# Kernel optimization log

Hardware: AMD Instinct MI355X
Metric: run time of the kernel (lower is better)

## Reference

```python
import jax, jax.numpy as jnp
import numpy as np

N_NODES = 1024
N_FEAT = 12        # must equal LOOKBACK (U1 @ B @ U2.T constraint in original code)
LOOKBACK = 12
N_DATA = 8
KSIZE = 2
DILATIONS = [1, 3, 3, 3]
DELTA_MIN = 0.05
TIME_FEATS = 36    # 15 + 5 + 4 + 12


def setup_inputs() -> dict:
    key = jax.random.key(0)
    ks = jax.random.split(key, 21)
    f32 = jnp.float32

    def rn(k, shape, fan_in):
        return jax.random.normal(k, shape, dtype=f32) / np.sqrt(fan_in)

    return {
        'observation': jax.random.normal(ks[0], (N_NODES, N_DATA, LOOKBACK), dtype=f32),
        'time_features': jax.random.normal(ks[1], (TIME_FEATS,), dtype=f32),
        # main FC stack: (n_nodes*n_data) -> fc1 -> fc2 -> n_nodes*n_feat
        'fc_w1': rn(ks[2], (N_NODES * N_DATA, 2048), N_NODES * N_DATA),
        'fc_b1': jnp.zeros((2048,), f32),
        'fc_w2': rn(ks[3], (2048, 2048), 2048),
        'fc_b2': jnp.zeros((2048,), f32),
        'fc_w3': rn(ks[4], (2048, N_NODES * N_FEAT), 2048),
        'fc_b3': jnp.zeros((N_NODES * N_FEAT,), f32),
        # graph conv weights
        'W_forward': rn(ks[5], (KSIZE, N_FEAT, N_FEAT), N_FEAT),
        'W_backward': rn(ks[6], (KSIZE, N_FEAT, N_FEAT), N_FEAT),
        'b': jnp.zeros((N_FEAT,), f32),
        # GraphConstructor params (one fixed set, reused for every adjacency)
        'layer_initial': rn(ks[7], (LOOKBACK, N_NODES), N_NODES),
        'gs_w1': rn(ks[8], (N_NODES, 256), N_NODES),
        'gs_b1': jnp.zeros((256,), f32),
        'gs_w2': rn(ks[9], (256, N_NODES * N_FEAT), 256),
        'gs_b2': jnp.zeros((N_NODES * N_FEAT,), f32),
        'gt_w1': rn(ks[10], (TIME_FEATS, 256), TIME_FEATS),
        'gt_b1': jnp.zeros((256,), f32),
        'gt_w2': rn(ks[11], (256, N_NODES * N_FEAT), 256),
        'gt_b2': jnp.zeros((N_NODES * N_FEAT,), f32),
        'B': jax.random.normal(ks[12], (N_FEAT, N_FEAT), dtype=f32) / N_FEAT,
    }


def _forward(observation, time_features, fc_w1, fc_b1, fc_w2, fc_b2, fc_w3, fc_b3,
             W_forward, W_backward, b, layer_initial,
             gs_w1, gs_b1, gs_w2, gs_b2, gt_w1, gt_b1, gt_w2, gt_b2, B):
    relu = jax.nn.relu

    # fully_connected: observation (N, D, L) -> X (N, F, L)
    obs = jnp.transpose(observation, (2, 0, 1)).reshape(LOOKBACK, -1)  # (L, N*D)
    h = relu(obs @ fc_w1 + fc_b1)
    h = relu(h @ fc_w2 + fc_b2)
    h = relu(h @ fc_w3 + fc_b3)                                        # (L, N*F)
    X0 = jnp.transpose(h.reshape(LOOKBACK, N_NODES, N_FEAT), (1, 2, 0))  # (N, F, L)

    # node embedding U (N, L, F), computed once (graph params fixed)
    sp = relu(relu(layer_initial @ gs_w1 + gs_b1) @ gs_w2 + gs_b2)     # (L, N*F)
    tp = relu(relu(time_features @ gt_w1 + gt_b1) @ gt_w2 + gt_b2)     # (N*F,)
    U = jnp.transpose((sp + tp).reshape(LOOKBACK, N_NODES, N_FEAT), (1, 0, 2))

    adj_cache = {}

    def norm_adj(a, c):
        # normalized adjacency between feature-slices a and c (static ints)
        if (a, c) in adj_cache:
            return adj_cache[(a, c)]
        U1 = U[:, :, a]                      # (N, L)
        U2 = U[:, :, c]                      # (N, L)
        x = U1 @ B @ U2.T                    # (N, N); valid since L == F
        x = jnp.where(x >= DELTA_MIN, x, 0.0)
        A = jax.nn.softmax(x, axis=1)        # torch F.softmax default dim=1 for 2D
        # degree = diag(rowsum); inv(sqrtm(diag)) = diag(1/sqrt(rowsum))
        d = 1.0 / jnp.sqrt(A.sum(-1))
        out = A * d[:, None] * d[None, :]
        adj_cache[(a, c)] = out
        return out

    def conv(X, t):
        Z = jnp.zeros((N_NODES, N_FEAT), jnp.float32)
        for k in range(KSIZE):
            X_t = X[:, :, t - k]             # (N, F)
            L1 = norm_adj(t - k, t)
            L2 = norm_adj(t + k, t)
            x = L1 @ X_t @ W_forward[k] + L2 @ X_t @ W_backward[k] + b
            Z = Z + jax.nn.relu(x)
        return Z

    def conv_layer(X, d):
        cols = []
        for t in range(1, LOOKBACK - 1):
            if t % d == 0:
                cols.append(conv(X, t))
            else:
                cols.append(jnp.zeros((N_NODES, N_FEAT), jnp.float32))
        return jnp.stack(cols, axis=-1)      # (N, F, L-2)

    Z0 = conv_layer(X0, DILATIONS[0])
    Z1 = conv_layer(Z0, DILATIONS[1])
    Z2 = conv_layer(Z1, DILATIONS[2])
    Z3 = conv_layer(Z2, DILATIONS[3])
    return (Z0[:, :, -1], Z1[:, :, -1], Z2[:, :, -1], Z3[:, :, -1])


def reference(observation, time_features, fc_w1, fc_b1, fc_w2, fc_b2, fc_w3, fc_b3,
              W_forward, W_backward, b, layer_initial,
              gs_w1, gs_b1, gs_w2, gs_b2, gt_w1, gt_b1, gt_w2, gt_b2, B):
    return _forward(observation, time_features, fc_w1, fc_b1, fc_w2, fc_b2, fc_w3, fc_b3,
                    W_forward, W_backward, b, layer_initial,
                    gs_w1, gs_b1, gs_w2, gs_b2, gt_w1, gt_b1, gt_w2, gt_b2, B)
```

## Files before the change

### kernel.cpp

```cpp
#include <hip/hip_runtime.h>

#define OFF_SPP   0
#define OFF_TPH   49152
#define OFF_P1    65536
#define OFF_P2    196608
#define OFF_P3    262144
#define OFF_UP    393216
#define OFF_TPP   1572864
#define OFF_U     1703936

template<int KS, int PIN, int P, int GATHER>
__device__ __forceinline__ void gemm_body(
    const float* __restrict__ xin, const float* __restrict__ bias_in,
    const float* __restrict__ W, float* __restrict__ part,
    int N, int K, int bx, int by, float* lx, float* red)
{
  int tid = threadIdx.x;
  int k0 = by * KS;
  for (int i = tid; i < 2*KS; i += 256) {
    int t = i / KS, kk = i - t*KS;
    float v;
    if (GATHER) {
      int k = k0 + kk;
      v = xin[(k >> 3)*96 + (k & 7)*12 + 9 + t];
    } else if (PIN == 0) {
      v = xin[t*K + k0 + kk];
    } else {
      v = 0.f;
      const float* p0 = xin + (size_t)(t*K + k0 + kk)*PIN;
      #pragma unroll
      for (int pp = 0; pp < PIN; ++pp) v += p0[pp];
    }
    if (bias_in) { v += bias_in[k0 + kk]; v = v > 0.f ? v : 0.f; }
    lx[i] = v;
  }
  __syncthreads();
  int kg = tid >> 5, cg2 = tid & 31;
  int colbase = bx*128 + cg2*4;
  float a0=0,a1=0,a2=0,a3=0,c0=0,c1=0,c2=0,c3=0;
  const int ksub = KS/8;
  for (int kk = kg*ksub; kk < kg*ksub + ksub; ++kk) {
    float4 w = *(const float4*)(W + (size_t)(k0+kk)*N + colbase);
    float x0 = lx[kk], x1 = lx[KS + kk];
    a0=fmaf(x0,w.x,a0); a1=fmaf(x0,w.y,a1); a2=fmaf(x0,w.z,a2); a3=fmaf(x0,w.w,a3);
    c0=fmaf(x1,w.x,c0); c1=fmaf(x1,w.y,c1); c2=fmaf(x1,w.z,c2); c3=fmaf(x1,w.w,c3);
  }
  float* rp = red + (kg*32 + cg2)*8;
  rp[0]=a0; rp[1]=a1; rp[2]=a2; rp[3]=a3; rp[4]=c0; rp[5]=c1; rp[6]=c2; rp[7]=c3;
  __syncthreads();
  int cg3 = tid & 31, q = tid >> 5;
  float s = 0.f;
  #pragma unroll
  for (int g = 0; g < 8; ++g) s += red[(g*32 + cg3)*8 + q];
  int t = q >> 2, c = q & 3;
  part[(size_t)(t*N + bx*128 + cg3*4 + c)*P + by] = s;
}

__global__ void __launch_bounds__(256) k_front(
    const float* __restrict__ obs, const float* __restrict__ fc_w1,
    float* __restrict__ part1,
    const float* __restrict__ li, const float* __restrict__ gs_w1,
    const float* __restrict__ tf, const float* __restrict__ gt_w1,
    const float* __restrict__ gt_b1,
    float* __restrict__ sp_part, float* __restrict__ tp_h,
    float* __restrict__ out_tail)
{
  __shared__ float smem[2560];
  int b = blockIdx.x, tid = threadIdx.x;
  if (b < 512) {
    gemm_body<256, 0, 32, 1>(obs, (const float*)nullptr, fc_w1, part1,
                             2048, 8192, b & 15, b >> 4, smem, smem + 512);
  } else if (b < 528) {
    float (*lil)[128] = (float(*)[128])smem;
    int sb = b - 512;
    int cb = sb & 1, kc = sb >> 1;
    for (int i = tid; i < 1536; i += 256) {
      int r = i >> 7, kk = i & 127;
      lil[r][kk] = li[r*1024 + kc*128 + kk];
    }
    __syncthreads();
    int col = cb*128 + (tid & 127);
    int kh = tid >> 7;
    float acc[12];
    #pragma unroll
    for (int t=0;t<12;++t) acc[t]=0.f;
    for (int kk = kh*64; kk < kh*64 + 64; ++kk) {
      float w = gs_w1[(size_t)(kc*128 + kk)*256 + col];
      #pragma unroll
      for (int t=0;t<12;++t) acc[t] = fmaf(lil[t][kk], w, acc[t]);
    }
    int c = kc*2 + kh;
    #pragma unroll
    for (int t=0;t<12;++t) sp_part[(c*12 + t)*256 + col] = acc[t];
    for (int i = tid; i < 2304; i += 256) out_tail[sb*2304 + i] = 0.f;
  } else {
    float acc = 0.f;
    for (int k = 0; k < 36; ++k)
      acc = fmaf(tf[k], gt_w1[k*256 + tid], acc);
    float v = acc + gt_b1[tid];
    tp_h[tid] = v > 0.f ? v : 0.f;
  }
}

__global__ void __launch_bounds__(256) k_umid(
    const float* __restrict__ part1, const float* __restrict__ fc_b1,
    const float* __restrict__ fc_w2, float* __restrict__ part2,
    const float* __restrict__ sp_part, const float* __restrict__ gs_b1,
    const float* __restrict__ tp_h,
    const float* __restrict__ gs_w2, const float* __restrict__ gt_w2,
    float* __restrict__ U_part, float* __restrict__ tp_part)
{
  __shared__ float smem[2304];
  int b = blockIdx.x, tid = threadIdx.x;
  if (b < 256) {
    gemm_body<128, 32, 16, 0>(part1, fc_b1, fc_w2, part2, 2048, 2048,
                              b & 15, b >> 4, smem, smem + 256);
    return;
  }
  float* spl = smem;
  float* tpl = smem + 96;
  int ug = b - 256;
  int n  = (ug & 3)*256 + tid;
  int uy = ug >> 2;
  int k0 = uy*8;
  if (tid < 96) {
    int kk = tid / 12, t = tid % 12;
    float v = gs_b1[k0 + kk];
    #pragma unroll
    for (int c = 0; c < 16; ++c) v += sp_part[(c*12 + t)*256 + k0 + kk];
    spl[kk*12 + t] = v > 0.f ? v : 0.f;
  }
  if (tid < 8) tpl[tid] = tp_h[k0 + tid];
  __syncthreads();
  float sA[3][12];
  float tA[3] = {0.f, 0.f, 0.f};
  #pragma unroll
  for (int ap=0;ap<3;++ap)
    #pragma unroll
    for (int t=0;t<12;++t) sA[ap][t]=0.f;
  #pragma unroll
  for (int kk = 0; kk < 8; ++kk) {
    float4 ws4 = *(const float4*)(gs_w2 + (size_t)(k0+kk)*12288 + 12*n + 8);
    float4 wt4 = *(const float4*)(gt_w2 + (size_t)(k0+kk)*12288 + 12*n + 8);
    float w0 = ws4.y, w1 = ws4.z, w2 = ws4.w;
    #pragma unroll
    for (int t=0;t<12;++t) {
      float s = spl[kk*12 + t];
      sA[0][t] = fmaf(s, w0, sA[0][t]);
      sA[1][t] = fmaf(s, w1, sA[1][t]);
      sA[2][t] = fmaf(s, w2, sA[2][t]);
    }
    float tv = tpl[kk];
    tA[0] = fmaf(tv, wt4.y, tA[0]);
    tA[1] = fmaf(tv, wt4.z, tA[1]);
    tA[2] = fmaf(tv, wt4.w, tA[2]);
  }
  #pragma unroll
  for (int ap=0;ap<3;++ap) {
    #pragma unroll
    for (int t=0;t<12;++t)
      U_part[(size_t)uy*36864 + ap*12288 + n*12 + t] = sA[ap][t];
    tp_part[uy*3072 + n*3 + ap] = tA[ap];
  }
}

__global__ void __launch_bounds__(256) k_fc3u(
    const float* __restrict__ part2, const float* __restrict__ fc_b2,
    const float* __restrict__ fc_w3, float* __restrict__ part3,
    const float* __restrict__ U_part, const float* __restrict__ tp_part,
    const float* __restrict__ gs_b2, const float* __restrict__ gt_b2,
    float* __restrict__ U)
{
  __shared__ float smem[3072];
  int b = blockIdx.x, tid = threadIdx.x;
  if (b < 384) {
    gemm_body<512, 16, 4, 0>(part2, fc_b2, fc_w3, part3, 12288, 2048,
                             b >> 2, b & 3, smem, smem + 1024);
    return;
  }
  int i = (b - 384)*256 + tid;
  float us = 0.f;
  for (int y = 0; y < 32; ++y) us += U_part[(size_t)y*36864 + i];
  int ap = i / 12288, rem = i - ap*12288, n = rem / 12;
  float ts = 0.f;
  for (int y = 0; y < 32; ++y) ts += tp_part[y*3072 + n*3 + ap];
  int c = n*12 + 9 + ap;
  float sv = us + gs_b2[c]; sv = sv > 0.f ? sv : 0.f;
  float tv = ts + gt_b2[c]; tv = tv > 0.f ? tv : 0.f;
  U[i] = sv + tv;
}

#define SS 1032
__global__ void __launch_bounds__(256) k_final(
    const float* __restrict__ U, const float* __restrict__ Bm,
    const float* __restrict__ part3, const float* __restrict__ fc_b3,
    const float* __restrict__ Wf, const float* __restrict__ Wb,
    const float* __restrict__ bvec, float* __restrict__ out)
{
  __shared__ float sc[6*SS];
  __shared__ float Pm[72];
  __shared__ float invS[6];
  __shared__ float Bl[144];
  __shared__ float Ws0[144], Ws1[144], Ws2[144];
  __shared__ float wbuf[72];
  __shared__ float bl[12];
  int tid = threadIdx.x;
  int i0 = blockIdx.x*2;
  if (tid < 144) {
    Bl[tid]  = Bm[tid];
    Ws0[tid] = Wf[144 + tid];
    Ws1[tid] = Wf[tid] + Wb[tid];
    Ws2[tid] = Wb[144 + tid];
  }
  if (tid < 12) bl[tid] = bvec[tid];
  __syncthreads();
  if (tid < 72) {
    int r = tid / 36, ap = (tid / 12) % 3, j = tid % 12;
    float s = 0.f;
    #pragma unroll
    for (int t=0;t<12;++t)
      s = fmaf(U[ap*12288 + (i0+r)*12 + t], Bl[t*12 + j], s);
    Pm[(r*3+ap)*12 + j] = s;
  }
  __syncthreads();
  const float* U10 = U + 12288;
  for (int jj = 0; jj < 4; ++jj) {
    int j = tid + jj*256;
    const float4* ur = (const float4*)(U10 + j*12);
    float4 u0 = ur[0], u1 = ur[1], u2 = ur[2];
    float u[12] = {u0.x,u0.y,u0.z,u0.w,u1.x,u1.y,u1.z,u1.w,u2.x,u2.y,u2.z,u2.w};
    #pragma unroll
    for (int r=0;r<2;++r)
      #pragma unroll
      for (int ap=0;ap<3;++ap) {
        float s = 0.f;
        #pragma unroll
        for (int t=0;t<12;++t) s = fmaf(Pm[(r*3+ap)*12 + t], u[t], s);
        sc[(r*3+ap)*SS + j] = (s >= 0.05f) ? s : 0.f;
      }
  }
  __syncthreads();
  int wv = tid >> 6, ln = tid & 63;
  for (int pr = wv; pr < 6; pr += 4) {
    float m = -1e30f;
    for (int q = 0; q < 16; ++q) m = fmaxf(m, sc[pr*SS + ln + q*64]);
    #pragma unroll
    for (int o = 32; o > 0; o >>= 1) m = fmaxf(m, __shfl_xor(m, o));
    float sum = 0.f;
    for (int q = 0; q < 16; ++q) {
      int j = ln + q*64;
      float e = __expf(sc[pr*SS + j] - m);
      sc[pr*SS + j] = e;
      sum += e;
    }
    #pragma unroll
    for (int o = 32; o > 0; o >>= 1) sum += __shfl_xor(sum, o);
    if (ln == 0) invS[pr] = 1.f / sum;
  }
  __syncthreads();
  float acc[2][12];
  #pragma unroll
  for (int r = 0; r < 2; ++r)
    #pragma unroll
    for (int f = 0; f < 12; ++f)
      acc[r][f] = 0.f;
  int q3 = tid >> 6, jg = tid & 63;
  if (tid < 192) {
    int row = (q3 == 1) ? 1 : 0;
    const float* p3r = part3 + (size_t)row*49152;
    for (int q = 0; q < 16; ++q) {
      int j = jg + q*64;
      float e0 = sc[q3*SS + j];
      float e1 = sc[(3 + q3)*SS + j];
      const float4* px = (const float4*)(p3r + (size_t)j*48);
      const float* bb = fc_b3 + j*12;
      #pragma unroll
      for (int f = 0; f < 12; ++f) {
        float4 v4 = px[f];
        float x = v4.x + v4.y + v4.z + v4.w + bb[f];
        x = x > 0.f ? x : 0.f;
        acc[0][f] = fmaf(e0, x, acc[0][f]);
        acc[1][f] = fmaf(e1, x, acc[1][f]);
      }
    }
  }
  __syncthreads();
  float* red = sc;
  if (tid < 192) {
    #pragma unroll
    for (int r=0;r<2;++r)
      #pragma unroll
      for (int f=0;f<12;++f)
        red[((q3*2 + r)*12 + f)*64 + jg] = acc[r][f];
  }
  __syncthreads();
  if (tid < 72) {
    int q3b = tid / 24, rr = (tid / 12) % 2, f = tid % 12;
    float s = 0.f;
    for (int g = 0; g < 64; ++g) s += red[((q3b*2 + rr)*12 + f)*64 + g];
    wbuf[(q3b*2 + rr)*12 + f] = s;
  }
  __syncthreads();
  if (tid < 24) {
    int r = tid / 12, g = tid % 12;
    float y0=0.f, y1=0.f, y2=0.f;
    #pragma unroll
    for (int f=0; f<12; ++f) {
      y0 = fmaf(wbuf[(0*2+r)*12+f], Ws0[f*12+g], y0);
      y1 = fmaf(wbuf[(1*2+r)*12+f], Ws1[f*12+g], y1);
      y2 = fmaf(wbuf[(2*2+r)*12+f], Ws2[f*12+g], y2);
    }
    float a1v = invS[r*3+1]*y1;
    float a2v = invS[r*3+0]*y0 + invS[r*3+2]*y2;
    float v1 = a1v + bl[g]; v1 = v1>0.f ? v1 : 0.f;
    float v2 = a2v + bl[g]; v2 = v2>0.f ? v2 : 0.f;
    out[(i0+r)*12 + g] = v1 + v2;
  }
}

extern "C" void kernel_launch(void* const* d_in, const int* in_sizes, int n_in,
                              void* d_out, int out_size, void* d_ws, size_t ws_size,
                              hipStream_t stream)
{
  const float* obs   = (const float*)d_in[0];
  const float* tf    = (const float*)d_in[1];
  const float* fc_w1 = (const float*)d_in[2];
  const float* fc_b1 = (const float*)d_in[3];
  const float* fc_w2 = (const float*)d_in[4];
  const float* fc_b2 = (const float*)d_in[5];
  const float* fc_w3 = (const float*)d_in[6];
  const float* fc_b3 = (const float*)d_in[7];
  const float* Wf    = (const float*)d_in[8];
  const float* Wb    = (const float*)d_in[9];
  const float* bvec  = (const float*)d_in[10];
  const float* li    = (const float*)d_in[11];
  const float* gs_w1 = (const float*)d_in[12];
  const float* gs_b1 = (const float*)d_in[13];
  const float* gs_w2 = (const float*)d_in[14];
  const float* gs_b2 = (const float*)d_in[15];
  const float* gt_w1 = (const float*)d_in[16];
  const float* gt_b1 = (const float*)d_in[17];
  const float* gt_w2 = (const float*)d_in[18];
  const float* gt_b2 = (const float*)d_in[19];
  const float* Bm    = (const float*)d_in[20];
  float* out = (float*)d_out;
  float* ws  = (float*)d_ws;

  float* sp_part = ws + OFF_SPP;
  float* tp_h    = ws + OFF_TPH;
  float* part1   = ws + OFF_P1;
  float* part2   = ws + OFF_P2;
  float* part3   = ws + OFF_P3;
  float* U_part  = ws + OFF_UP;
  float* tp_part = ws + OFF_TPP;
  float* U       = ws + OFF_U;

  k_front<<<dim3(529), dim3(256), 0, stream>>>(obs, fc_w1, part1,
                                               li, gs_w1, tf, gt_w1, gt_b1,
                                               sp_part, tp_h, out + 12288);
  k_umid<<<dim3(384), dim3(256), 0, stream>>>(part1, fc_b1, fc_w2, part2,
                                              sp_part, gs_b1, tp_h,
                                              gs_w2, gt_w2, U_part, tp_part);
  k_fc3u<<<dim3(528), dim3(256), 0, stream>>>(part2, fc_b2, fc_w3, part3,
                                              U_part, tp_part, gs_b2, gt_b2, U);
  k_final<<<dim3(512), dim3(256), 0, stream>>>(U, Bm, part3, fc_b3,
                                               Wf, Wb, bvec, out);
}
```

Baseline: 305.4 us.

## Deepen split-K across FC GEMMs and reduce fc3 via atomics into bias-initialized buffer

Each of the three FC GEMMs now uses a smaller K chunk, which roughly doubles or quadruples the block count and spreads the weight streaming over more workgroups. The fc3 GEMM no longer writes per-chunk partials. It atomically adds into an X buffer that k_front pre-fills with fc_b3, so k_final reads a single reduced row instead of summing four partials plus the bias. The trade is more partial-sum traffic for fc1 and fc2, plus atomic contention and nondeterministic float summation order in fc3.

```diff
diff --git a/kernel.cpp b/kernel.cpp
--- a/kernel.cpp
+++ b/kernel.cpp
@@ -3,13 +3,13 @@
 #define OFF_SPP   0
 #define OFF_TPH   49152
 #define OFF_P1    65536
-#define OFF_P2    196608
-#define OFF_P3    262144
-#define OFF_UP    393216
-#define OFF_TPP   1572864
-#define OFF_U     1703936
-
-template<int KS, int PIN, int P, int GATHER>
+#define OFF_P2    327680
+#define OFF_X     458752
+#define OFF_UP    524288
+#define OFF_TPP   1703936
+#define OFF_U     1802240
+
+template<int KS, int PIN, int P, int GATHER, int ATOM>
 __device__ __forceinline__ void gemm_body(
     const float* __restrict__ xin, const float* __restrict__ bias_in,
     const float* __restrict__ W, float* __restrict__ part,
@@ -53,7 +53,11 @@
   #pragma unroll
   for (int g = 0; g < 8; ++g) s += red[(g*32 + cg3)*8 + q];
   int t = q >> 2, c = q & 3;
-  part[(size_t)(t*N + bx*128 + cg3*4 + c)*P + by] = s;
+  if (ATOM) {
+    atomicAdd(part + (size_t)t*N + bx*128 + cg3*4 + c, s);
+  } else {
+    part[(size_t)(t*N + bx*128 + cg3*4 + c)*P + by] = s;
+  }
 }
 
 __global__ void __launch_bounds__(256) k_front(
@@ -61,18 +65,18 @@
     float* __restrict__ part1,
     const float* __restrict__ li, const float* __restrict__ gs_w1,
     const float* __restrict__ tf, const float* __restrict__ gt_w1,
-    const float* __restrict__ gt_b1,
+    const float* __restrict__ gt_b1, const float* __restrict__ fc_b3,
     float* __restrict__ sp_part, float* __restrict__ tp_h,
-    float* __restrict__ out_tail)
-{
-  __shared__ float smem[2560];
+    float* __restrict__ X_raw, float* __restrict__ out_tail)
+{
+  __shared__ float smem[2304];
   int b = blockIdx.x, tid = threadIdx.x;
-  if (b < 512) {
-    gemm_body<256, 0, 32, 1>(obs, (const float*)nullptr, fc_w1, part1,
-                             2048, 8192, b & 15, b >> 4, smem, smem + 512);
-  } else if (b < 528) {
+  if (b < 1024) {
+    gemm_body<128, 0, 64, 1, 0>(obs, (const float*)nullptr, fc_w1, part1,
+                                2048, 8192, b & 15, b >> 4, smem, smem + 256);
+  } else if (b < 1040) {
     float (*lil)[128] = (float(*)[128])smem;
-    int sb = b - 512;
+    int sb = b - 1024;
     int cb = sb & 1, kc = sb >> 1;
     for (int i = tid; i < 1536; i += 256) {
       int r = i >> 7, kk = i & 127;
@@ -93,6 +97,11 @@
     #pragma unroll
     for (int t=0;t<12;++t) sp_part[(c*12 + t)*256 + col] = acc[t];
     for (int i = tid; i < 2304; i += 256) out_tail[sb*2304 + i] = 0.f;
+    for (int i = tid; i < 1536; i += 256) {
+      int idx = sb*1536 + i;
+      int colx = idx >= 12288 ? idx - 12288 : idx;
+      X_raw[idx] = fc_b3[colx];
+    }
   } else {
     float acc = 0.f;
     for (int k = 0; k < 36; ++k)
@@ -110,16 +119,16 @@
     const float* __restrict__ gs_w2, const float* __restrict__ gt_w2,
     float* __restrict__ U_part, float* __restrict__ tp_part)
 {
-  __shared__ float smem[2304];
+  __shared__ float smem[2176];
   int b = blockIdx.x, tid = threadIdx.x;
-  if (b < 256) {
-    gemm_body<128, 32, 16, 0>(part1, fc_b1, fc_w2, part2, 2048, 2048,
-                              b & 15, b >> 4, smem, smem + 256);
+  if (b < 512) {
+    gemm_body<64, 64, 32, 0, 0>(part1, fc_b1, fc_w2, part2, 2048, 2048,
+                                b & 15, b >> 4, smem, smem + 128);
     return;
   }
   float* spl = smem;
   float* tpl = smem + 96;
-  int ug = b - 256;
+  int ug = b - 512;
   int n  = (ug & 3)*256 + tid;
   int uy = ug >> 2;
   int k0 = uy*8;
@@ -166,19 +175,19 @@
 
 __global__ void __launch_bounds__(256) k_fc3u(
     const float* __restrict__ part2, const float* __restrict__ fc_b2,
-    const float* __restrict__ fc_w3, float* __restrict__ part3,
+    const float* __restrict__ fc_w3, float* __restrict__ X_raw,
     const float* __restrict__ U_part, const float* __restrict__ tp_part,
     const float* __restrict__ gs_b2, const float* __restrict__ gt_b2,
     float* __restrict__ U)
 {
-  __shared__ float smem[3072];
+  __shared__ float smem[2304];
   int b = blockIdx.x, tid = threadIdx.x;
-  if (b < 384) {
-    gemm_body<512, 16, 4, 0>(part2, fc_b2, fc_w3, part3, 12288, 2048,
-                             b >> 2, b & 3, smem, smem + 1024);
+  if (b < 1536) {
+    gemm_body<128, 32, 0, 0, 1>(part2, fc_b2, fc_w3, X_raw, 12288, 2048,
+                                b >> 4, b & 15, smem, smem + 256);
     return;
   }
-  int i = (b - 384)*256 + tid;
+  int i = (b - 1536)*256 + tid;
   float us = 0.f;
   for (int y = 0; y < 32; ++y) us += U_part[(size_t)y*36864 + i];
   int ap = i / 12288, rem = i - ap*12288, n = rem / 12;
@@ -193,7 +202,7 @@
 #define SS 1032
 __global__ void __launch_bounds__(256) k_final(
     const float* __restrict__ U, const float* __restrict__ Bm,
-    const float* __restrict__ part3, const float* __restrict__ fc_b3,
+    const float* __restrict__ X_raw,
     const float* __restrict__ Wf, const float* __restrict__ Wb,
     const float* __restrict__ bvec, float* __restrict__ out)
 {
@@ -267,18 +276,17 @@
   int q3 = tid >> 6, jg = tid & 63;
   if (tid < 192) {
     int row = (q3 == 1) ? 1 : 0;
-    const float* p3r = part3 + (size_t)row*49152;
+    const float* xr = X_raw + (size_t)row*12288;
     for (int q = 0; q < 16; ++q) {
       int j = jg + q*64;
       float e0 = sc[q3*SS + j];
       float e1 = sc[(3 + q3)*SS + j];
-      const float4* px = (const float4*)(p3r + (size_t)j*48);
-      const float* bb = fc_b3 + j*12;
+      const float4* px = (const float4*)(xr + j*12);
+      float4 v0 = px[0], v1 = px[1], v2 = px[2];
+      float xv[12] = {v0.x,v0.y,v0.z,v0.w,v1.x,v1.y,v1.z,v1.w,v2.x,v2.y,v2.z,v2.w};
       #pragma unroll
       for (int f = 0; f < 12; ++f) {
-        float4 v4 = px[f];
-        float x = v4.x + v4.y + v4.z + v4.w + bb[f];
-        x = x > 0.f ? x : 0.f;
+        float x = xv[f] > 0.f ? xv[f] : 0.f;
         acc[0][f] = fmaf(e0, x, acc[0][f]);
         acc[1][f] = fmaf(e1, x, acc[1][f]);
       }
@@ -350,19 +358,21 @@
   float* tp_h    = ws + OFF_TPH;
   float* part1   = ws + OFF_P1;
   float* part2   = ws + OFF_P2;
-  float* part3   = ws + OFF_P3;
+  float* X_raw   = ws + OFF_X;
   float* U_part  = ws + OFF_UP;
   float* tp_part = ws + OFF_TPP;
   float* U       = ws + OFF_U;
 
-  k_front<<<dim3(529), dim3(256), 0, stream>>>(obs, fc_w1, part1,
-                                               li, gs_w1, tf, gt_w1, gt_b1,
-                                               sp_part, tp_h, out + 12288);
-  k_umid<<<dim3(384), dim3(256), 0, stream>>>(part1, fc_b1, fc_w2, part2,
+  k_front<<<dim3(1041), dim3(256), 0, stream>>>(obs, fc_w1, part1,
+                                                li, gs_w1, tf, gt_w1, gt_b1,
+                                                fc_b3, sp_part, tp_h,
+                                                X_raw, out + 12288);
+  k_umid<<<dim3(640), dim3(256), 0, stream>>>(part1, fc_b1, fc_w2, part2,
                                               sp_part, gs_b1, tp_h,
                                               gs_w2, gt_w2, U_part, tp_part);
-  k_fc3u<<<dim3(528), dim3(256), 0, stream>>>(part2, fc_b2, fc_w3, part3,
-                                              U_part, tp_part, gs_b2, gt_b2, U);
-  k_final<<<dim3(512), dim3(256), 0, stream>>>(U, Bm, part3, fc_b3,
+  k_fc3u<<<dim3(1680), dim3(256), 0, stream>>>(part2, fc_b2, fc_w3, X_raw,
+                                               U_part, tp_part, gs_b2, gt_b2,
+                                               U);
+  k_final<<<dim3(512), dim3(256), 0, stream>>>(U, Bm, X_raw,
                                                Wf, Wb, bvec, out);
 }
```

New measurement: 291.9 us. -4.4%, faster.
